# Kernel tuning notes

Hardware: AMD Instinct MI355X
Metric: run time of the kernel (lower is better)

## Reference

```python
import jax, jax.numpy as jnp
import numpy as np

B, T, D, H, C = 128, 256, 256, 1024, 1000

def _xavier(k, shape):
    std = (2.0 / (shape[0] + shape[1])) ** 0.5
    return jax.random.normal(k, shape, dtype=jnp.float32) * std

def setup_inputs() -> dict:
    key = jax.random.key(0)
    ks = jax.random.split(key, 10)
    inp = {"x": jax.random.normal(ks[0], (B, T, D), dtype=jnp.float32)}
    for n, k in zip(["W_gx", "W_ix", "W_fx", "W_ox"], ks[1:5]):
        inp[n] = _xavier(k, (D, H))
    for n, k in zip(["W_gh", "W_ih", "W_fh", "W_oh"], ks[5:9]):
        inp[n] = _xavier(k, (H, H))
    inp["W_ph"] = _xavier(ks[9], (H, C))
    for n in ["b_g", "b_i", "b_f", "b_o"]:
        inp[n] = jnp.zeros((H,), dtype=jnp.float32)
    inp["b_p"] = jnp.zeros((C,), dtype=jnp.float32)
    return inp

def reference(x, W_gx, W_ix, W_fx, W_ox, W_gh, W_ih, W_fh, W_oh, W_ph,
              b_g, b_i, b_f, b_o, b_p):
    b, t, d = x.shape
    h_dim = W_gh.shape[0]
    # Precompute all input projections in batched GEMMs: [T, B, H]
    xg = jnp.einsum('btd,dh->tbh', x, W_gx) + b_g
    xi = jnp.einsum('btd,dh->tbh', x, W_ix) + b_i
    xf = jnp.einsum('btd,dh->tbh', x, W_fx) + b_f
    xo = jnp.einsum('btd,dh->tbh', x, W_ox) + b_o

    def step(carry, xs):
        h, c = carry
        pg, pi, pf, po = xs
        g = jnp.tanh(pg + h @ W_gh)
        i = jax.nn.sigmoid(pi + h @ W_ih)
        f = jax.nn.sigmoid(pf + h @ W_fh)
        o = jax.nn.sigmoid(po + h @ W_oh)
        c = g * i + c * f
        h = jnp.tanh(c) * o
        return (h, c), None

    h0 = jnp.zeros((b, h_dim), dtype=x.dtype)
    c0 = jnp.zeros((b, h_dim), dtype=x.dtype)
    (h_T, _), _ = jax.lax.scan(step, (h0, c0), (xg, xi, xf, xo))
    p = h_T @ W_ph + b_p  # [B, num_classes]
    return jax.nn.log_softmax(p, axis=1)
```

## Files before the change

### kernel.cpp

```cpp
#include <hip/hip_runtime.h>
#include <hip/hip_bf16.h>

#define B_ 128
#define T_ 256
#define D_ 256
#define H_ 1024
#define C_ 1000

typedef __attribute__((ext_vector_type(8))) short short8;
typedef __attribute__((ext_vector_type(4))) float floatx4;

static __device__ __forceinline__ unsigned short f2bf(float f) {
  unsigned int u = __builtin_bit_cast(unsigned int, f);
  u += 0x7fffu + ((u >> 16) & 1u);
  return (unsigned short)(u >> 16);
}
static __device__ __forceinline__ float bf2f(unsigned short s) {
  unsigned int u = ((unsigned int)s) << 16;
  return __builtin_bit_cast(float, u);
}
static __device__ __forceinline__ float sigm(float z) {
  return 1.0f / (1.0f + __expf(-z));
}
static __device__ __forceinline__ float tanh_fast(float z) {
  z = fminf(fmaxf(z, -15.f), 15.f);
  float e = __expf(2.f * z);
  return (e - 1.f) / (e + 1.f);
}

__global__ __launch_bounds__(256) void pack_all(
    const float* __restrict__ Wgx, const float* __restrict__ Wix,
    const float* __restrict__ Wfx, const float* __restrict__ Wox,
    const float* __restrict__ Wgh, const float* __restrict__ Wih,
    const float* __restrict__ Wfh, const float* __restrict__ Woh,
    unsigned short* __restrict__ Wp,
    const float* __restrict__ x, unsigned short* __restrict__ xb) {
  int blk = blockIdx.x;
  if (blk < 2560) {
    int t = blk * 256 + threadIdx.x;
    int L = t & 63;
    int g = (t >> 6) & 3;
    int rest = t >> 8;
    int kc = rest % 40;
    int jb = rest / 40;
    int n = L & 15, q = L >> 4;
    int j = jb * 16 + n;
    const float* Wh = (g == 0) ? Wgh : (g == 1) ? Wih : (g == 2) ? Wfh : Woh;
    const float* Wx = (g == 0) ? Wgx : (g == 1) ? Wix : (g == 2) ? Wfx : Wox;
    int k0 = kc * 32 + q * 8;
    unsigned int w[4];
#pragma unroll
    for (int i = 0; i < 4; i++) {
      int ka = k0 + 2 * i, kb = k0 + 2 * i + 1;
      float fa = (ka < H_) ? Wh[(size_t)ka * H_ + j] : Wx[(size_t)(ka - H_) * H_ + j];
      float fb = (kb < H_) ? Wh[(size_t)kb * H_ + j] : Wx[(size_t)(kb - H_) * H_ + j];
      w[i] = (unsigned int)f2bf(fa) | ((unsigned int)f2bf(fb) << 16);
    }
    uint4 v = {w[0], w[1], w[2], w[3]};
    *((uint4*)(Wp + (size_t)t * 8)) = v;
  } else {
    int idx = (blk - 2560) * 256 + threadIdx.x;
    int d8 = idx & 31;
    int tt = (idx >> 5) & 255;
    int b = idx >> 13;
    const float* src = x + ((size_t)b * T_ + tt) * D_ + d8 * 8;
    int rt = b >> 4, kcx = d8 >> 2, q = d8 & 3, m = b & 15;
    size_t dst = ((((size_t)tt * 8 + rt) * 8 + kcx) * 64 + (q * 16 + m)) * 8;
    unsigned int w[4];
#pragma unroll
    for (int i = 0; i < 4; i++) {
      float fa = src[2 * i], fb = src[2 * i + 1];
      w[i] = (unsigned int)f2bf(fa) | ((unsigned int)f2bf(fb) << 16);
    }
    uint4 v = {w[0], w[1], w[2], w[3]};
    *((uint4*)(xb + dst)) = v;
  }
}

__global__ __launch_bounds__(256, 1) void lstm_all(
    unsigned short* __restrict__ hb0, unsigned short* __restrict__ hb1,
    const unsigned short* __restrict__ Wp, const unsigned short* __restrict__ xb,
    const float* __restrict__ bg, const float* __restrict__ bi,
    const float* __restrict__ bf_, const float* __restrict__ bo,
    unsigned int* __restrict__ fl) {
  __shared__ unsigned short WL[32 * 4 * 64 * 8];
  __shared__ float xg[2][4][32][17];
  __shared__ float bb[4][16];

  const int tid = threadIdx.x;
  const int bid = blockIdx.x;
  const int jb = bid >> 2, rtq = bid & 3;
  const int w = tid >> 6, lane = tid & 63;
  const int rt01 = w & 1, kh = w >> 1;
  const int rt = rtq * 2 + rt01;
  const int grp = rtq * 64;

  (void)__hip_atomic_load(&fl[0], __ATOMIC_ACQUIRE, __HIP_MEMORY_SCOPE_AGENT);

  {
    const uint4* src = (const uint4*)(Wp + (size_t)jb * (40 * 4 * 64 * 8));
    uint4* dst = (uint4*)WL;
#pragma unroll
    for (int i = 0; i < 32; i++) dst[i * 256 + tid] = src[i * 256 + tid];
  }
  if (tid < 64) {
    int g = tid >> 4, n = tid & 15;
    const float* bs = (g == 0) ? bg : (g == 1) ? bi : (g == 2) ? bf_ : bo;
    bb[g][n] = bs[jb * 16 + n];
  }
  {
    int rr = tid >> 3, n0 = (tid & 7) * 2;
    int r = rtq * 32 + rr;
    int rt_r = r >> 4, m = r & 15;
    int j = jb * 16 + n0;
    size_t dst = ((size_t)(rt_r * 32 + (j >> 5)) * 64 + (((j >> 3) & 3) * 16 + m)) * 8 + (j & 7);
    __hip_atomic_store((unsigned int*)(hb0 + dst), 0u, __ATOMIC_RELAXED,
                       __HIP_MEMORY_SCOPE_AGENT);
  }
  float c0 = 0.f, c1 = 0.f;

  const short8* BpX = (const short8*)Wp + (size_t)jb * (40 * 4 * 64) + lane;
  const short8* BL = (const short8*)WL + (size_t)kh * 4096 + lane;
  const int kc0 = kh * 16;
  const int kx0 = kh * 4;

  short8 bxw[4][4];
#pragma unroll
  for (int i = 0; i < 4; i++)
#pragma unroll
    for (int g = 0; g < 4; g++)
      bxw[i][g] = BpX[(size_t)((32 + kx0 + i) * 4 + g) * 64];

  __syncthreads();

  if (tid == 0)
    __hip_atomic_store(&fl[grp + jb], 1u, __ATOMIC_RELAXED, __HIP_MEMORY_SCOPE_AGENT);

  floatx4 xa0 = {0.f, 0.f, 0.f, 0.f};
  floatx4 xa1 = xa0, xa2 = xa0, xa3 = xa0;
  {
    const short8* Ax = (const short8*)xb + ((size_t)rt * 8 + kx0) * 64 + lane;
    short8 ax[4];
#pragma unroll
    for (int i = 0; i < 4; i++) ax[i] = Ax[(size_t)i * 64];
#pragma unroll
    for (int i = 0; i < 4; i++) {
      xa0 = __builtin_amdgcn_mfma_f32_16x16x32_bf16(ax[i], bxw[i][0], xa0, 0, 0, 0);
      xa1 = __builtin_amdgcn_mfma_f32_16x16x32_bf16(ax[i], bxw[i][1], xa1, 0, 0, 0);
      xa2 = __builtin_amdgcn_mfma_f32_16x16x32_bf16(ax[i], bxw[i][2], xa2, 0, 0, 0);
      xa3 = __builtin_amdgcn_mfma_f32_16x16x32_bf16(ax[i], bxw[i][3], xa3, 0, 0, 0);
    }
  }

#pragma unroll 1
  for (int t = 0; t < 256; t++) {
    const unsigned short* hc = (t & 1) ? hb1 : hb0;
    unsigned short* hn = (t & 1) ? hb0 : hb1;

    short8 pb0[16], pb1[16];
#pragma unroll
    for (int i = 0; i < 16; i++) {
      pb0[i] = BL[(size_t)(i * 4 + 0) * 64];
      pb1[i] = BL[(size_t)(i * 4 + 1) * 64];
    }

    {
      unsigned int tgt = (unsigned int)t + 1u;
      while (true) {
        unsigned int v = __hip_atomic_load(&fl[grp + kh * 32 + (lane & 31)],
                                           __ATOMIC_RELAXED, __HIP_MEMORY_SCOPE_AGENT);
        if (__all((int)(v >= tgt))) break;
      }
    }
    asm volatile("" ::: "memory");

    const unsigned short* Ahp = hc + ((size_t)(rt * 32 + kc0) * 64 + lane) * 8;
    unsigned long long hq[32];
#pragma unroll
    for (int i = 0; i < 16; i++) {
      hq[2 * i] = __hip_atomic_load((const unsigned long long*)(Ahp + (size_t)i * 512),
                                    __ATOMIC_RELAXED, __HIP_MEMORY_SCOPE_AGENT);
      hq[2 * i + 1] = __hip_atomic_load((const unsigned long long*)(Ahp + (size_t)i * 512 + 4),
                                        __ATOMIC_RELAXED, __HIP_MEMORY_SCOPE_AGENT);
    }

    floatx4 a0 = xa0, a1 = xa1, a2 = xa2, a3 = xa3;
#pragma unroll
    for (int kc = 0; kc < 16; kc++) {
      union { unsigned long long q[2]; short8 v; } u;
      u.q[0] = hq[2 * kc];
      u.q[1] = hq[2 * kc + 1];
      short8 av = u.v;
      short8 b2 = BL[(size_t)(kc * 4 + 2) * 64];
      short8 b3 = BL[(size_t)(kc * 4 + 3) * 64];
      a0 = __builtin_amdgcn_mfma_f32_16x16x32_bf16(av, pb0[kc], a0, 0, 0, 0);
      a1 = __builtin_amdgcn_mfma_f32_16x16x32_bf16(av, pb1[kc], a1, 0, 0, 0);
      a2 = __builtin_amdgcn_mfma_f32_16x16x32_bf16(av, b2, a2, 0, 0, 0);
      a3 = __builtin_amdgcn_mfma_f32_16x16x32_bf16(av, b3, a3, 0, 0, 0);
    }

    {
      int cl = lane & 15, q = lane >> 4;
#pragma unroll
      for (int p = 0; p < 4; p++) {
        int rrow = rt01 * 16 + q * 4 + p;
        xg[kh][0][rrow][cl] = a0[p];
        xg[kh][1][rrow][cl] = a1[p];
        xg[kh][2][rrow][cl] = a2[p];
        xg[kh][3][rrow][cl] = a3[p];
      }
    }
    int tn = (t < 255) ? t + 1 : 255;
    const short8* Axn = (const short8*)xb + (((size_t)tn * 8 + rt) * 8 + kx0) * 64 + lane;
    short8 ax[4];
#pragma unroll
    for (int i = 0; i < 4; i++) ax[i] = Axn[(size_t)i * 64];

    __syncthreads();

    {
      int rr = tid >> 3, n0 = (tid & 7) * 2;
      int r = rtq * 32 + rr;
      int rt_r = r >> 4, m = r & 15;
      unsigned int packed = 0;
#pragma unroll
      for (int u = 0; u < 2; u++) {
        int n = n0 + u;
        float pg = xg[0][0][rr][n] + xg[1][0][rr][n] + bb[0][n];
        float pi_ = xg[0][1][rr][n] + xg[1][1][rr][n] + bb[1][n];
        float pf = xg[0][2][rr][n] + xg[1][2][rr][n] + bb[2][n];
        float po = xg[0][3][rr][n] + xg[1][3][rr][n] + bb[3][n];
        float gg = tanh_fast(pg);
        float ii = sigm(pi_);
        float ff = sigm(pf);
        float oo = sigm(po);
        float cold = u ? c1 : c0;
        float cn = gg * ii + cold * ff;
        if (u) c1 = cn; else c0 = cn;
        float hv = tanh_fast(cn) * oo;
        packed |= ((unsigned int)f2bf(hv)) << (16 * u);
      }
      int j = jb * 16 + n0;
      size_t dst = ((size_t)(rt_r * 32 + (j >> 5)) * 64 + (((j >> 3) & 3) * 16 + m)) * 8 + (j & 7);
      __hip_atomic_store((unsigned int*)(hn + dst), packed, __ATOMIC_RELAXED,
                         __HIP_MEMORY_SCOPE_AGENT);
    }
    __syncthreads();

    if (t < 255) {
      if (tid == 0)
        __hip_atomic_store(&fl[grp + jb], (unsigned int)t + 2u, __ATOMIC_RELAXED,
                           __HIP_MEMORY_SCOPE_AGENT);

      xa0 = (floatx4){0.f, 0.f, 0.f, 0.f};
      xa1 = xa0; xa2 = xa0; xa3 = xa0;
#pragma unroll
      for (int i = 0; i < 4; i++) {
        xa0 = __builtin_amdgcn_mfma_f32_16x16x32_bf16(ax[i], bxw[i][0], xa0, 0, 0, 0);
        xa1 = __builtin_amdgcn_mfma_f32_16x16x32_bf16(ax[i], bxw[i][1], xa1, 0, 0, 0);
        xa2 = __builtin_amdgcn_mfma_f32_16x16x32_bf16(ax[i], bxw[i][2], xa2, 0, 0, 0);
        xa3 = __builtin_amdgcn_mfma_f32_16x16x32_bf16(ax[i], bxw[i][3], xa3, 0, 0, 0);
      }
    }
  }
}

__global__ __launch_bounds__(256) void proj_mfma(const unsigned short* __restrict__ hB,
                                                 const float* __restrict__ Wph,
                                                 const float* __restrict__ bp,
                                                 float* __restrict__ Lbuf) {
  __shared__ float pacc[4][16][17];
  const int tid = threadIdx.x;
  const int rt = blockIdx.x & 7;
  const int cb = blockIdx.x >> 3;
  const int w = tid >> 6, lane = tid & 63;
  const int n = lane & 15, q = lane >> 4;
  const int j = cb * 16 + n;
  const bool jv = (j < C_);

  floatx4 acc = {0.f, 0.f, 0.f, 0.f};
  const short8* Ah = (const short8*)hB + ((size_t)rt * 32) * 64 + lane;
#pragma unroll
  for (int kq = 0; kq < 8; kq++) {
    int kc = w * 8 + kq;
    short8 a = Ah[(size_t)kc * 64];
    int k0 = kc * 32 + q * 8;
    unsigned int wb[4];
#pragma unroll
    for (int i = 0; i < 4; i++) {
      float fa = jv ? Wph[(size_t)(k0 + 2 * i) * C_ + j] : 0.f;
      float fb = jv ? Wph[(size_t)(k0 + 2 * i + 1) * C_ + j] : 0.f;
      wb[i] = (unsigned int)f2bf(fa) | ((unsigned int)f2bf(fb) << 16);
    }
    union { unsigned int u[4]; short8 v; } bu;
    bu.u[0] = wb[0]; bu.u[1] = wb[1]; bu.u[2] = wb[2]; bu.u[3] = wb[3];
    acc = __builtin_amdgcn_mfma_f32_16x16x32_bf16(a, bu.v, acc, 0, 0, 0);
  }
#pragma unroll
  for (int p = 0; p < 4; p++) pacc[w][q * 4 + p][n] = acc[p];
  __syncthreads();

  {
    int r = tid >> 4, nn = tid & 15;
    int jj = cb * 16 + nn;
    float s = pacc[0][r][nn] + pacc[1][r][nn] + pacc[2][r][nn] + pacc[3][r][nn];
    s += (jj < C_) ? bp[jj] : 0.f;
    Lbuf[(size_t)(rt * 16 + r) * 1008 + jj] = s;
  }
}

__global__ __launch_bounds__(256) void softmax_k(const float* __restrict__ Lbuf,
                                                 float* __restrict__ out) {
  __shared__ float red[256];
  int row = blockIdx.x, tid = threadIdx.x;
  const float* Lr = Lbuf + (size_t)row * 1008;
  bool v3 = (tid + 768 < C_);
  float a0 = Lr[tid];
  float a1 = Lr[tid + 256];
  float a2 = Lr[tid + 512];
  float a3 = v3 ? Lr[tid + 768] : 0.f;

  float mx = fmaxf(fmaxf(a0, a1), a2);
  if (v3) mx = fmaxf(mx, a3);
  red[tid] = mx;
  __syncthreads();
  for (int s = 128; s > 0; s >>= 1) {
    if (tid < s) red[tid] = fmaxf(red[tid], red[tid + s]);
    __syncthreads();
  }
  float M = red[0];
  __syncthreads();
  float se = __expf(a0 - M) + __expf(a1 - M) + __expf(a2 - M);
  if (v3) se += __expf(a3 - M);
  red[tid] = se;
  __syncthreads();
  for (int s = 128; s > 0; s >>= 1) {
    if (tid < s) red[tid] += red[tid + s];
    __syncthreads();
  }
  float lse = M + logf(red[0]);
  out[(size_t)row * C_ + tid] = a0 - lse;
  out[(size_t)row * C_ + tid + 256] = a1 - lse;
  out[(size_t)row * C_ + tid + 512] = a2 - lse;
  if (v3) out[(size_t)row * C_ + tid + 768] = a3 - lse;
}

extern "C" void kernel_launch(void* const* d_in, const int* in_sizes, int n_in,
                              void* d_out, int out_size, void* d_ws, size_t ws_size,
                              hipStream_t stream) {
  const float* x   = (const float*)d_in[0];
  const float* Wgx = (const float*)d_in[1];
  const float* Wix = (const float*)d_in[2];
  const float* Wfx = (const float*)d_in[3];
  const float* Wox = (const float*)d_in[4];
  const float* Wgh = (const float*)d_in[5];
  const float* Wih = (const float*)d_in[6];
  const float* Wfh = (const float*)d_in[7];
  const float* Woh = (const float*)d_in[8];
  const float* Wph = (const float*)d_in[9];
  const float* bg  = (const float*)d_in[10];
  const float* bi  = (const float*)d_in[11];
  const float* bf  = (const float*)d_in[12];
  const float* bo  = (const float*)d_in[13];
  const float* bp  = (const float*)d_in[14];

  char* ws = (char*)d_ws;
  unsigned short* Wp = (unsigned short*)ws;
  size_t off = 10485760;
  unsigned short* xb = (unsigned short*)(ws + off);
  float* Lbuf = (float*)xb;
  off += 16777216;
  unsigned short* hb0 = (unsigned short*)(ws + off); off += 262144;
  unsigned short* hb1 = (unsigned short*)(ws + off); off += 262144;
  unsigned int* fl = (unsigned int*)(ws + off); off += 4096;

  hipMemsetAsync(fl, 0, 4096, stream);

  pack_all<<<6656, 256, 0, stream>>>(Wgx, Wix, Wfx, Wox, Wgh, Wih, Wfh, Woh, Wp, x, xb);

  void* args[] = {(void*)&hb0, (void*)&hb1, (void*)&Wp, (void*)&xb,
                  (void*)&bg, (void*)&bi, (void*)&bf, (void*)&bo, (void*)&fl};
  hipError_t cerr = hipLaunchCooperativeKernel((void*)lstm_all, dim3(256), dim3(256),
                                               args, 0, stream);
  if (cerr != hipSuccess) {
    lstm_all<<<256, 256, 0, stream>>>(hb0, hb1, Wp, xb, bg, bi, bf, bo, fl);
  }

  proj_mfma<<<504, 256, 0, stream>>>(hb0, Wph, bp, Lbuf);
  softmax_k<<<128, 256, 0, stream>>>(Lbuf, (float*)d_out);
}
```

Measured before the change: 1.141 ms.

## Replace per-step flag barrier with sentinel-filled hidden-state ring buffer

Allocates a 257-slot ring of hidden-state buffers, pre-filled with a NaN sentinel bf16 pattern (slot 0 zeroed), so consumers poll the h data itself and retry until no sentinel remains. This removes the separate flag store/poll round trip and the trailing block barrier per timestep. The cost is filling about 67 MB with sentinels in the pack kernel and reloading all of h on each retry. It also drops the register-prefetched weight fragments and falls back to the old flag path when the workspace is too small.

```diff
diff --git a/kernel.cpp b/kernel.cpp
--- a/kernel.cpp
+++ b/kernel.cpp
@@ -6,6 +6,7 @@
 #define D_ 256
 #define H_ 1024
 #define C_ 1000
+#define SENT 0x7F81u
 
 typedef __attribute__((ext_vector_type(8))) short short8;
 typedef __attribute__((ext_vector_type(4))) float floatx4;
@@ -34,7 +35,8 @@
     const float* __restrict__ Wgh, const float* __restrict__ Wih,
     const float* __restrict__ Wfh, const float* __restrict__ Woh,
     unsigned short* __restrict__ Wp,
-    const float* __restrict__ x, unsigned short* __restrict__ xb) {
+    const float* __restrict__ x, unsigned short* __restrict__ xb,
+    unsigned short* __restrict__ hring) {
   int blk = blockIdx.x;
   if (blk < 2560) {
     int t = blk * 256 + threadIdx.x;
@@ -58,7 +60,7 @@
     }
     uint4 v = {w[0], w[1], w[2], w[3]};
     *((uint4*)(Wp + (size_t)t * 8)) = v;
-  } else {
+  } else if (blk < 6656) {
     int idx = (blk - 2560) * 256 + threadIdx.x;
     int d8 = idx & 31;
     int tt = (idx >> 5) & 255;
@@ -74,15 +76,21 @@
     }
     uint4 v = {w[0], w[1], w[2], w[3]};
     *((uint4*)(xb + dst)) = v;
+  } else {
+    size_t g = (size_t)(blk - 6656) * 256 + threadIdx.x;
+    size_t byte = g * 16;
+    unsigned int v = (byte < 262144) ? 0u : (SENT | (SENT << 16));
+    uint4 q = {v, v, v, v};
+    *((uint4*)((char*)hring + byte)) = q;
   }
 }
 
 __global__ __launch_bounds__(256, 1) void lstm_all(
-    unsigned short* __restrict__ hb0, unsigned short* __restrict__ hb1,
+    unsigned short* __restrict__ hring, unsigned short* __restrict__ hb1,
     const unsigned short* __restrict__ Wp, const unsigned short* __restrict__ xb,
     const float* __restrict__ bg, const float* __restrict__ bi,
     const float* __restrict__ bf_, const float* __restrict__ bo,
-    unsigned int* __restrict__ fl) {
+    unsigned int* __restrict__ fl, int ring) {
   __shared__ unsigned short WL[32 * 4 * 64 * 8];
   __shared__ float xg[2][4][32][17];
   __shared__ float bb[4][16];
@@ -108,13 +116,13 @@
     const float* bs = (g == 0) ? bg : (g == 1) ? bi : (g == 2) ? bf_ : bo;
     bb[g][n] = bs[jb * 16 + n];
   }
-  {
+  if (!ring) {
     int rr = tid >> 3, n0 = (tid & 7) * 2;
     int r = rtq * 32 + rr;
     int rt_r = r >> 4, m = r & 15;
     int j = jb * 16 + n0;
     size_t dst = ((size_t)(rt_r * 32 + (j >> 5)) * 64 + (((j >> 3) & 3) * 16 + m)) * 8 + (j & 7);
-    __hip_atomic_store((unsigned int*)(hb0 + dst), 0u, __ATOMIC_RELAXED,
+    __hip_atomic_store((unsigned int*)(hring + dst), 0u, __ATOMIC_RELAXED,
                        __HIP_MEMORY_SCOPE_AGENT);
   }
   float c0 = 0.f, c1 = 0.f;
@@ -133,7 +141,7 @@
 
   __syncthreads();
 
-  if (tid == 0)
+  if (!ring && tid == 0)
     __hip_atomic_store(&fl[grp + jb], 1u, __ATOMIC_RELAXED, __HIP_MEMORY_SCOPE_AGENT);
 
   floatx4 xa0 = {0.f, 0.f, 0.f, 0.f};
@@ -152,114 +160,216 @@
     }
   }
 
+  if (ring) {
 #pragma unroll 1
-  for (int t = 0; t < 256; t++) {
-    const unsigned short* hc = (t & 1) ? hb1 : hb0;
-    unsigned short* hn = (t & 1) ? hb0 : hb1;
-
-    short8 pb0[16], pb1[16];
-#pragma unroll
-    for (int i = 0; i < 16; i++) {
-      pb0[i] = BL[(size_t)(i * 4 + 0) * 64];
-      pb1[i] = BL[(size_t)(i * 4 + 1) * 64];
+    for (int t = 0; t < 256; t++) {
+      const unsigned short* hc = hring + (size_t)t * 131072;
+      unsigned short* hn = hring + (size_t)(t + 1) * 131072;
+      const unsigned short* Ahp = hc + ((size_t)(rt * 32 + kc0) * 64 + lane) * 8;
+
+      unsigned long long hq[32];
+      while (true) {
+        bool bad = false;
+#pragma unroll
+        for (int i = 0; i < 16; i++) {
+          unsigned long long qa = __hip_atomic_load(
+              (const unsigned long long*)(Ahp + (size_t)i * 512),
+              __ATOMIC_RELAXED, __HIP_MEMORY_SCOPE_AGENT);
+          unsigned long long qb = __hip_atomic_load(
+              (const unsigned long long*)(Ahp + (size_t)i * 512 + 4),
+              __ATOMIC_RELAXED, __HIP_MEMORY_SCOPE_AGENT);
+          hq[2 * i] = qa;
+          hq[2 * i + 1] = qb;
+          bad |= ((qa & 0xFFFFull) == SENT) | (((qa >> 32) & 0xFFFFull) == SENT) |
+                 ((qb & 0xFFFFull) == SENT) | (((qb >> 32) & 0xFFFFull) == SENT);
+        }
+        if (!__any((int)bad)) break;
+      }
+      asm volatile("" ::: "memory");
+
+      floatx4 a0 = xa0, a1 = xa1, a2 = xa2, a3 = xa3;
+#pragma unroll
+      for (int kc = 0; kc < 16; kc++) {
+        union { unsigned long long q[2]; short8 v; } u;
+        u.q[0] = hq[2 * kc];
+        u.q[1] = hq[2 * kc + 1];
+        short8 av = u.v;
+        short8 b0 = BL[(size_t)(kc * 4 + 0) * 64];
+        short8 b1v = BL[(size_t)(kc * 4 + 1) * 64];
+        short8 b2 = BL[(size_t)(kc * 4 + 2) * 64];
+        short8 b3 = BL[(size_t)(kc * 4 + 3) * 64];
+        a0 = __builtin_amdgcn_mfma_f32_16x16x32_bf16(av, b0, a0, 0, 0, 0);
+        a1 = __builtin_amdgcn_mfma_f32_16x16x32_bf16(av, b1v, a1, 0, 0, 0);
+        a2 = __builtin_amdgcn_mfma_f32_16x16x32_bf16(av, b2, a2, 0, 0, 0);
+        a3 = __builtin_amdgcn_mfma_f32_16x16x32_bf16(av, b3, a3, 0, 0, 0);
+      }
+
+      __syncthreads();
+
+      {
+        int cl = lane & 15, q = lane >> 4;
+#pragma unroll
+        for (int p = 0; p < 4; p++) {
+          int rrow = rt01 * 16 + q * 4 + p;
+          xg[kh][0][rrow][cl] = a0[p];
+          xg[kh][1][rrow][cl] = a1[p];
+          xg[kh][2][rrow][cl] = a2[p];
+          xg[kh][3][rrow][cl] = a3[p];
+        }
+      }
+      int tn = (t < 255) ? t + 1 : 255;
+      const short8* Axn = (const short8*)xb + (((size_t)tn * 8 + rt) * 8 + kx0) * 64 + lane;
+      short8 ax[4];
+#pragma unroll
+      for (int i = 0; i < 4; i++) ax[i] = Axn[(size_t)i * 64];
+
+      __syncthreads();
+
+      {
+        int rr = tid >> 3, n0 = (tid & 7) * 2;
+        int r = rtq * 32 + rr;
+        int rt_r = r >> 4, m = r & 15;
+        unsigned int packed = 0;
+#pragma unroll
+        for (int u = 0; u < 2; u++) {
+          int n = n0 + u;
+          float pg = xg[0][0][rr][n] + xg[1][0][rr][n] + bb[0][n];
+          float pi_ = xg[0][1][rr][n] + xg[1][1][rr][n] + bb[1][n];
+          float pf = xg[0][2][rr][n] + xg[1][2][rr][n] + bb[2][n];
+          float po = xg[0][3][rr][n] + xg[1][3][rr][n] + bb[3][n];
+          float gg = tanh_fast(pg);
+          float ii = sigm(pi_);
+          float ff = sigm(pf);
+          float oo = sigm(po);
+          float cold = u ? c1 : c0;
+          float cn = gg * ii + cold * ff;
+          if (u) c1 = cn; else c0 = cn;
+          float hv = tanh_fast(cn) * oo;
+          packed |= ((unsigned int)f2bf(hv)) << (16 * u);
+        }
+        int j = jb * 16 + n0;
+        size_t dst = ((size_t)(rt_r * 32 + (j >> 5)) * 64 + (((j >> 3) & 3) * 16 + m)) * 8 + (j & 7);
+        __hip_atomic_store((unsigned int*)(hn + dst), packed, __ATOMIC_RELAXED,
+                           __HIP_MEMORY_SCOPE_AGENT);
+      }
+
+      if (t < 255) {
+        xa0 = (floatx4){0.f, 0.f, 0.f, 0.f};
+        xa1 = xa0; xa2 = xa0; xa3 = xa0;
+#pragma unroll
+        for (int i = 0; i < 4; i++) {
+          xa0 = __builtin_amdgcn_mfma_f32_16x16x32_bf16(ax[i], bxw[i][0], xa0, 0, 0, 0);
+          xa1 = __builtin_amdgcn_mfma_f32_16x16x32_bf16(ax[i], bxw[i][1], xa1, 0, 0, 0);
+          xa2 = __builtin_amdgcn_mfma_f32_16x16x32_bf16(ax[i], bxw[i][2], xa2, 0, 0, 0);
+          xa3 = __builtin_amdgcn_mfma_f32_16x16x32_bf16(ax[i], bxw[i][3], xa3, 0, 0, 0);
+        }
+      }
     }
-
-    {
-      unsigned int tgt = (unsigned int)t + 1u;
-      while (true) {
-        unsigned int v = __hip_atomic_load(&fl[grp + kh * 32 + (lane & 31)],
-                                           __ATOMIC_RELAXED, __HIP_MEMORY_SCOPE_AGENT);
-        if (__all((int)(v >= tgt))) break;
-      }
-    }
-    asm volatile("" ::: "memory");
-
-    const unsigned short* Ahp = hc + ((size_t)(rt * 32 + kc0) * 64 + lane) * 8;
-    unsigned long long hq[32];
-#pragma unroll
-    for (int i = 0; i < 16; i++) {
-      hq[2 * i] = __hip_atomic_load((const unsigned long long*)(Ahp + (size_t)i * 512),
-                                    __ATOMIC_RELAXED, __HIP_MEMORY_SCOPE_AGENT);
-      hq[2 * i + 1] = __hip_atomic_load((const unsigned long long*)(Ahp + (size_t)i * 512 + 4),
-                                        __ATOMIC_RELAXED, __HIP_MEMORY_SCOPE_AGENT);
-    }
-
-    floatx4 a0 = xa0, a1 = xa1, a2 = xa2, a3 = xa3;
-#pragma unroll
-    for (int kc = 0; kc < 16; kc++) {
-      union { unsigned long long q[2]; short8 v; } u;
-      u.q[0] = hq[2 * kc];
-      u.q[1] = hq[2 * kc + 1];
-      short8 av = u.v;
-      short8 b2 = BL[(size_t)(kc * 4 + 2) * 64];
-      short8 b3 = BL[(size_t)(kc * 4 + 3) * 64];
-      a0 = __builtin_amdgcn_mfma_f32_16x16x32_bf16(av, pb0[kc], a0, 0, 0, 0);
-      a1 = __builtin_amdgcn_mfma_f32_16x16x32_bf16(av, pb1[kc], a1, 0, 0, 0);
-      a2 = __builtin_amdgcn_mfma_f32_16x16x32_bf16(av, b2, a2, 0, 0, 0);
-      a3 = __builtin_amdgcn_mfma_f32_16x16x32_bf16(av, b3, a3, 0, 0, 0);
-    }
-
-    {
-      int cl = lane & 15, q = lane >> 4;
-#pragma unroll
-      for (int p = 0; p < 4; p++) {
-        int rrow = rt01 * 16 + q * 4 + p;
-        xg[kh][0][rrow][cl] = a0[p];
-        xg[kh][1][rrow][cl] = a1[p];
-        xg[kh][2][rrow][cl] = a2[p];
-        xg[kh][3][rrow][cl] = a3[p];
-      }
-    }
-    int tn = (t < 255) ? t + 1 : 255;
-    const short8* Axn = (const short8*)xb + (((size_t)tn * 8 + rt) * 8 + kx0) * 64 + lane;
-    short8 ax[4];
-#pragma unroll
-    for (int i = 0; i < 4; i++) ax[i] = Axn[(size_t)i * 64];
-
-    __syncthreads();
-
-    {
-      int rr = tid >> 3, n0 = (tid & 7) * 2;
-      int r = rtq * 32 + rr;
-      int rt_r = r >> 4, m = r & 15;
-      unsigned int packed = 0;
-#pragma unroll
-      for (int u = 0; u < 2; u++) {
-        int n = n0 + u;
-        float pg = xg[0][0][rr][n] + xg[1][0][rr][n] + bb[0][n];
-        float pi_ = xg[0][1][rr][n] + xg[1][1][rr][n] + bb[1][n];
-        float pf = xg[0][2][rr][n] + xg[1][2][rr][n] + bb[2][n];
-        float po = xg[0][3][rr][n] + xg[1][3][rr][n] + bb[3][n];
-        float gg = tanh_fast(pg);
-        float ii = sigm(pi_);
-        float ff = sigm(pf);
-        float oo = sigm(po);
-        float cold = u ? c1 : c0;
-        float cn = gg * ii + cold * ff;
-        if (u) c1 = cn; else c0 = cn;
-        float hv = tanh_fast(cn) * oo;
-        packed |= ((unsigned int)f2bf(hv)) << (16 * u);
-      }
-      int j = jb * 16 + n0;
-      size_t dst = ((size_t)(rt_r * 32 + (j >> 5)) * 64 + (((j >> 3) & 3) * 16 + m)) * 8 + (j & 7);
-      __hip_atomic_store((unsigned int*)(hn + dst), packed, __ATOMIC_RELAXED,
-                         __HIP_MEMORY_SCOPE_AGENT);
-    }
-    __syncthreads();
-
-    if (t < 255) {
-      if (tid == 0)
-        __hip_atomic_store(&fl[grp + jb], (unsigned int)t + 2u, __ATOMIC_RELAXED,
+  } else {
+#pragma unroll 1
+    for (int t = 0; t < 256; t++) {
+      const unsigned short* hc = (t & 1) ? hb1 : hring;
+      unsigned short* hn = (t & 1) ? hring : hb1;
+
+      {
+        unsigned int tgt = (unsigned int)t + 1u;
+        while (true) {
+          unsigned int v = __hip_atomic_load(&fl[grp + kh * 32 + (lane & 31)],
+                                             __ATOMIC_RELAXED, __HIP_MEMORY_SCOPE_AGENT);
+          if (__all((int)(v >= tgt))) break;
+        }
+      }
+      asm volatile("" ::: "memory");
+
+      const unsigned short* Ahp = hc + ((size_t)(rt * 32 + kc0) * 64 + lane) * 8;
+      unsigned long long hq[32];
+#pragma unroll
+      for (int i = 0; i < 16; i++) {
+        hq[2 * i] = __hip_atomic_load((const unsigned long long*)(Ahp + (size_t)i * 512),
+                                      __ATOMIC_RELAXED, __HIP_MEMORY_SCOPE_AGENT);
+        hq[2 * i + 1] = __hip_atomic_load((const unsigned long long*)(Ahp + (size_t)i * 512 + 4),
+                                          __ATOMIC_RELAXED, __HIP_MEMORY_SCOPE_AGENT);
+      }
+
+      floatx4 a0 = xa0, a1 = xa1, a2 = xa2, a3 = xa3;
+#pragma unroll
+      for (int kc = 0; kc < 16; kc++) {
+        union { unsigned long long q[2]; short8 v; } u;
+        u.q[0] = hq[2 * kc];
+        u.q[1] = hq[2 * kc + 1];
+        short8 av = u.v;
+        short8 b0 = BL[(size_t)(kc * 4 + 0) * 64];
+        short8 b1v = BL[(size_t)(kc * 4 + 1) * 64];
+        short8 b2 = BL[(size_t)(kc * 4 + 2) * 64];
+        short8 b3 = BL[(size_t)(kc * 4 + 3) * 64];
+        a0 = __builtin_amdgcn_mfma_f32_16x16x32_bf16(av, b0, a0, 0, 0, 0);
+        a1 = __builtin_amdgcn_mfma_f32_16x16x32_bf16(av, b1v, a1, 0, 0, 0);
+        a2 = __builtin_amdgcn_mfma_f32_16x16x32_bf16(av, b2, a2, 0, 0, 0);
+        a3 = __builtin_amdgcn_mfma_f32_16x16x32_bf16(av, b3, a3, 0, 0, 0);
+      }
+
+      __syncthreads();
+      {
+        int cl = lane & 15, q = lane >> 4;
+#pragma unroll
+        for (int p = 0; p < 4; p++) {
+          int rrow = rt01 * 16 + q * 4 + p;
+          xg[kh][0][rrow][cl] = a0[p];
+          xg[kh][1][rrow][cl] = a1[p];
+          xg[kh][2][rrow][cl] = a2[p];
+          xg[kh][3][rrow][cl] = a3[p];
+        }
+      }
+      int tn = (t < 255) ? t + 1 : 255;
+      const short8* Axn = (const short8*)xb + (((size_t)tn * 8 + rt) * 8 + kx0) * 64 + lane;
+      short8 ax[4];
+#pragma unroll
+      for (int i = 0; i < 4; i++) ax[i] = Axn[(size_t)i * 64];
+
+      __syncthreads();
+
+      {
+        int rr = tid >> 3, n0 = (tid & 7) * 2;
+        int r = rtq * 32 + rr;
+        int rt_r = r >> 4, m = r & 15;
+        unsigned int packed = 0;
+#pragma unroll
+        for (int u = 0; u < 2; u++) {
+          int n = n0 + u;
+          float pg = xg[0][0][rr][n] + xg[1][0][rr][n] + bb[0][n];
+          float pi_ = xg[0][1][rr][n] + xg[1][1][rr][n] + bb[1][n];
+          float pf = xg[0][2][rr][n] + xg[1][2][rr][n] + bb[2][n];
+          float po = xg[0][3][rr][n] + xg[1][3][rr][n] + bb[3][n];
+          float gg = tanh_fast(pg);
+          float ii = sigm(pi_);
+          float ff = sigm(pf);
+          float oo = sigm(po);
+          float cold = u ? c1 : c0;
+          float cn = gg * ii + cold * ff;
+          if (u) c1 = cn; else c0 = cn;
+          float hv = tanh_fast(cn) * oo;
+          packed |= ((unsigned int)f2bf(hv)) << (16 * u);
+        }
+        int j = jb * 16 + n0;
+        size_t dst = ((size_t)(rt_r * 32 + (j >> 5)) * 64 + (((j >> 3) & 3) * 16 + m)) * 8 + (j & 7);
+        __hip_atomic_store((unsigned int*)(hn + dst), packed, __ATOMIC_RELAXED,
                            __HIP_MEMORY_SCOPE_AGENT);
-
-      xa0 = (floatx4){0.f, 0.f, 0.f, 0.f};
-      xa1 = xa0; xa2 = xa0; xa3 = xa0;
-#pragma unroll
-      for (int i = 0; i < 4; i++) {
-        xa0 = __builtin_amdgcn_mfma_f32_16x16x32_bf16(ax[i], bxw[i][0], xa0, 0, 0, 0);
-        xa1 = __builtin_amdgcn_mfma_f32_16x16x32_bf16(ax[i], bxw[i][1], xa1, 0, 0, 0);
-        xa2 = __builtin_amdgcn_mfma_f32_16x16x32_bf16(ax[i], bxw[i][2], xa2, 0, 0, 0);
-        xa3 = __builtin_amdgcn_mfma_f32_16x16x32_bf16(ax[i], bxw[i][3], xa3, 0, 0, 0);
+      }
+      __syncthreads();
+
+      if (t < 255) {
+        if (tid == 0)
+          __hip_atomic_store(&fl[grp + jb], (unsigned int)t + 2u, __ATOMIC_RELAXED,
+                             __HIP_MEMORY_SCOPE_AGENT);
+        xa0 = (floatx4){0.f, 0.f, 0.f, 0.f};
+        xa1 = xa0; xa2 = xa0; xa3 = xa0;
+#pragma unroll
+        for (int i = 0; i < 4; i++) {
+          xa0 = __builtin_amdgcn_mfma_f32_16x16x32_bf16(ax[i], bxw[i][0], xa0, 0, 0, 0);
+          xa1 = __builtin_amdgcn_mfma_f32_16x16x32_bf16(ax[i], bxw[i][1], xa1, 0, 0, 0);
+          xa2 = __builtin_amdgcn_mfma_f32_16x16x32_bf16(ax[i], bxw[i][2], xa2, 0, 0, 0);
+          xa3 = __builtin_amdgcn_mfma_f32_16x16x32_bf16(ax[i], bxw[i][3], xa3, 0, 0, 0);
+        }
       }
     }
   }
@@ -370,22 +480,42 @@
   unsigned short* xb = (unsigned short*)(ws + off);
   float* Lbuf = (float*)xb;
   off += 16777216;
-  unsigned short* hb0 = (unsigned short*)(ws + off); off += 262144;
-  unsigned short* hb1 = (unsigned short*)(ws + off); off += 262144;
-  unsigned int* fl = (unsigned int*)(ws + off); off += 4096;
+
+  const size_t ring_bytes = 257ull * 262144ull;
+  const size_t ring_need = off + ring_bytes + 4096ull;
+  int ring = (ws_size >= ring_need) ? 1 : 0;
+
+  unsigned short* hbase;
+  unsigned short* hb1;
+  unsigned short* hfin;
+  unsigned int* fl;
+  if (ring) {
+    hbase = (unsigned short*)(ws + off); off += ring_bytes;
+    hb1 = hbase;
+    hfin = hbase + 256ull * 131072ull;
+    fl = (unsigned int*)(ws + off); off += 4096;
+  } else {
+    hbase = (unsigned short*)(ws + off); off += 262144;
+    hb1 = (unsigned short*)(ws + off); off += 262144;
+    hfin = hbase;
+    fl = (unsigned int*)(ws + off); off += 4096;
+  }
 
   hipMemsetAsync(fl, 0, 4096, stream);
 
-  pack_all<<<6656, 256, 0, stream>>>(Wgx, Wix, Wfx, Wox, Wgh, Wih, Wfh, Woh, Wp, x, xb);
-
-  void* args[] = {(void*)&hb0, (void*)&hb1, (void*)&Wp, (void*)&xb,
-                  (void*)&bg, (void*)&bi, (void*)&bf, (void*)&bo, (void*)&fl};
+  int pack_blocks = ring ? (6656 + 16448) : 6656;
+  pack_all<<<pack_blocks, 256, 0, stream>>>(Wgx, Wix, Wfx, Wox, Wgh, Wih, Wfh, Woh,
+                                            Wp, x, xb, hbase);
+
+  void* args[] = {(void*)&hbase, (void*)&hb1, (void*)&Wp, (void*)&xb,
+                  (void*)&bg, (void*)&bi, (void*)&bf, (void*)&bo, (void*)&fl,
+                  (void*)&ring};
   hipError_t cerr = hipLaunchCooperativeKernel((void*)lstm_all, dim3(256), dim3(256),
                                                args, 0, stream);
   if (cerr != hipSuccess) {
-    lstm_all<<<256, 256, 0, stream>>>(hb0, hb1, Wp, xb, bg, bi, bf, bo, fl);
-  }
-
-  proj_mfma<<<504, 256, 0, stream>>>(hb0, Wph, bp, Lbuf);
+    lstm_all<<<256, 256, 0, stream>>>(hbase, hb1, Wp, xb, bg, bi, bf, bo, fl, ring);
+  }
+
+  proj_mfma<<<504, 256, 0, stream>>>(hfin, Wph, bp, Lbuf);
   softmax_k<<<128, 256, 0, stream>>>(Lbuf, (float*)d_out);
 }
```

Result: slower. 1.325 ms (+16.1%).
